# Kernel tuning notes

Measured on AMD Instinct MI355X. Metric: run time of the kernel, lower is better.

Reference implementation:

```python
import jax, jax.numpy as jnp
import numpy as np

N = 100000      # nodes
E = 1200000     # edges (every node gets >=1 incoming edge)
DIN = 64
DOUT = 64
EDIM = 16
AVG_D = 2.5649493574615367  # log(avg_in_degree + 1) = log(13)
EPS = 1e-5


def setup_inputs() -> dict:
    key = jax.random.key(0)
    ks = jax.random.split(key, 10)
    h = jax.random.normal(ks[0], (N, DIN), dtype=jnp.float32)
    e = jax.random.normal(ks[1], (E, EDIM), dtype=jnp.float32)
    snorm_n = jax.random.uniform(ks[2], (N, 1), dtype=jnp.float32, minval=0.05, maxval=1.0)
    src = jax.random.randint(ks[3], (E,), 0, N, dtype=jnp.int32)
    # guarantee in-degree >= 1 for every node (DGL reduce requires non-empty mailbox)
    dst = jnp.concatenate([jnp.arange(N, dtype=jnp.int32),
                           jax.random.randint(ks[4], (E - N,), 0, N, dtype=jnp.int32)])
    d_pre_in = 2 * DIN + EDIM  # 144
    d_post_in = (4 * 3 + 1) * DIN  # 832
    W_pre = jax.random.normal(ks[5], (d_pre_in, DIN), dtype=jnp.float32) / np.sqrt(d_pre_in)
    b_pre = jnp.zeros((DIN,), dtype=jnp.float32)
    W_post = jax.random.normal(ks[6], (d_post_in, DOUT), dtype=jnp.float32) / np.sqrt(d_post_in)
    b_post = jnp.zeros((DOUT,), dtype=jnp.float32)
    bn_gamma = jnp.ones((DOUT,), dtype=jnp.float32)
    bn_beta = jnp.zeros((DOUT,), dtype=jnp.float32)
    return {"h": h, "e": e, "snorm_n": snorm_n,
            "W_pre": W_pre, "b_pre": b_pre, "W_post": W_post, "b_post": b_post,
            "bn_gamma": bn_gamma, "bn_beta": bn_beta, "src": src, "dst": dst}


def reference(h, e, snorm_n, W_pre, b_pre, W_post, b_post, bn_gamma, bn_beta, src, dst):
    n = h.shape[0]
    # --- pretrans on edges: MLP(cat[src_feat, dst_feat, edge_feat]) (1 layer, no act) ---
    z = jnp.concatenate([h[src], h[dst], e], axis=1)           # [E, 2*DIN+EDIM]
    m = z @ W_pre + b_pre                                      # [E, DIN] edge messages
    # --- multi-aggregator segment reduce over destination mailboxes ---
    deg = jax.ops.segment_sum(jnp.ones((m.shape[0],), m.dtype), dst, num_segments=n)
    D = deg[:, None]                                           # [N,1], all >= 1
    s1 = jax.ops.segment_sum(m, dst, num_segments=n)
    s2 = jax.ops.segment_sum(m * m, dst, num_segments=n)
    mean = s1 / D
    std = jnp.sqrt(jax.nn.relu(s2 / D - mean * mean) + EPS)
    mx = jax.ops.segment_max(m, dst, num_segments=n)
    mn = jax.ops.segment_min(m, dst, num_segments=n)
    agg = jnp.concatenate([mean, mx, mn, std], axis=1)          # [N, 4*DIN]
    # --- degree scalers: identity, amplification, attenuation ---
    logd = jnp.log(D + 1.0)
    scaled = jnp.concatenate([agg, agg * (logd / AVG_D), agg * (AVG_D / logd)], axis=1)  # [N, 12*DIN]
    # --- posttrans on cat[h, aggregated] (1 layer, no act) ---
    feat = jnp.concatenate([h, scaled], axis=1)                 # [N, 13*DIN]
    out = feat @ W_post + b_post                                # [N, DOUT]
    out = out * snorm_n                                        # graph norm
    # BatchNorm1d in training mode (batch stats over nodes, biased var)
    mu = out.mean(axis=0)
    var = out.var(axis=0)
    out = (out - mu) / jnp.sqrt(var + 1e-5) * bn_gamma + bn_beta
    # dropout p=0.0 -> identity
    return out
```

## Files before the change

kernel.cpp:

```cpp
#include <hip/hip_runtime.h>
#include <hip/hip_bf16.h>
#include <math.h>

#define N_NODES 100000
#define N_EDGES 1200000
#define NT_EDGE 75000
#define NPASS   3
#define TILES_PER_PASS 25000
#define ROWS_PER_PASS  400000
#define NT_POST 6250
#define AVG_D   2.5649493574615367f
#define EPSV    1e-5f

#define BUK_SHIFT 9
#define NBUK 196
#define EB_PER_BLOCK 4096

typedef __attribute__((ext_vector_type(8))) short short8;
typedef __attribute__((ext_vector_type(4))) float f32x4;

struct ERec { unsigned eid, sn, dn; };

#define OFF_DEG       0u
#define OFF_ROWLOCAL  400000u
#define OFF_BSUM      800000u
#define OFF_BOFFS     802048u
#define OFF_ROWSTART  804096u
#define OFF_CURSOR    1204096u
#define OFF_EREC      1604096u
#define OFF_AB        16004096u
#define OFF_BNACC     16804096u
#define OFF_BNFIN     16804608u
#define OFF_HB        16805120u
#define OFF_MBUF      29605120u
#define OFF_AGG       80805120u
#define OFF_WFRAG     132005120u
#define OFF_WFRAG2    132025600u
#define OFF_CARRY     OFF_BSUM
#define OFF_STAGING   OFF_MBUF
#define OFF_OUTPRE    OFF_MBUF

__device__ __forceinline__ short f2b(float f){
    union { float f; unsigned u; } c; c.f = f;
    unsigned u = c.u;
    unsigned r = (u + 0x7fffu + ((u >> 16) & 1u)) >> 16;
    return (short)r;
}
__device__ __forceinline__ float b2f(unsigned u16){
    union { unsigned u; float f; } c; c.u = u16 << 16;
    return c.f;
}
__device__ __forceinline__ unsigned pk(float a, float b){
    return ((unsigned)(unsigned short)f2b(a)) | (((unsigned)(unsigned short)f2b(b)) << 16);
}

__global__ void k_prep(const int* __restrict__ dst, unsigned* __restrict__ deg,
                       const float* __restrict__ h, unsigned short* __restrict__ hb,
                       const float* __restrict__ W_pre, unsigned short* __restrict__ wfrag,
                       const float* __restrict__ W_post, unsigned short* __restrict__ wfrag2){
    int i = blockIdx.x*256 + threadIdx.x;
    if (i < N_EDGES) atomicAdd(&deg[dst[i]], 1u);
    if (i < 800000){
        const float4* p = (const float4*)h + (size_t)i*2;
        float4 u0 = p[0], u1 = p[1];
        uint4 o;
        o.x = pk(u0.x,u0.y); o.y = pk(u0.z,u0.w);
        o.z = pk(u1.x,u1.y); o.w = pk(u1.z,u1.w);
        ((uint4*)hb)[i] = o;
    }
    if (i < 10240){
        int e = i & 7, l = (i>>3) & 63, q = i>>9;
        int ks = q>>2, cg = q&3;
        int lr = l&15, lg = l>>4;
        int k = ks*32 + lg*8 + e, col = cg*16 + lr;
        wfrag[i] = (unsigned short)((k < 144) ? f2b(W_pre[k*64 + col]) : (short)0);
    }
    if (i < 53248){
        int e = i & 7, l = (i>>3) & 63, g = i>>9;
        int cg = g & 3, f = g>>2;
        int lr = l&15, lg = l>>4;
        int col = cg*16 + lr;
        int row;
        if      (f < 10) row = f*32        + lg*8 + e;
        else if (f < 18) row = 320 + (f-10)*32 + lg*8 + e;
        else             row = 576 + (f-18)*32 + lg*8 + e;
        wfrag2[i] = (unsigned short)f2b(W_post[row*64 + col]);
    }
}
__global__ void k_scan1(const unsigned* __restrict__ deg, unsigned* __restrict__ rowlocal,
                        unsigned* __restrict__ bsum){
    __shared__ unsigned s[256];
    int t = threadIdx.x; int i = blockIdx.x*256 + t;
    unsigned d = (i < N_NODES) ? deg[i] : 0u;
    s[t] = d; __syncthreads();
    for (int off=1; off<256; off<<=1){
        unsigned v = (t>=off) ? s[t-off] : 0u; __syncthreads();
        s[t] += v; __syncthreads();
    }
    if (i < N_NODES) rowlocal[i] = s[t] - d;
    if (t == 255) bsum[blockIdx.x] = s[255];
}
__global__ void k_scan2(const unsigned* __restrict__ bsum, unsigned* __restrict__ boffs){
    __shared__ unsigned s[512];
    int t = threadIdx.x;
    unsigned v = (t < 391) ? bsum[t] : 0u;
    s[t] = v; __syncthreads();
    for (int off=1; off<512; off<<=1){
        unsigned x = (t>=off) ? s[t-off] : 0u; __syncthreads();
        s[t] += x; __syncthreads();
    }
    boffs[t] = s[t] - v;
}
__global__ void k_scan3(const unsigned* __restrict__ rowlocal, const unsigned* __restrict__ boffs,
                        unsigned* __restrict__ rowstart, unsigned* __restrict__ bukCursor){
    int i = blockIdx.x*256 + threadIdx.x;
    if (i < N_NODES){
        unsigned v = rowlocal[i] + boffs[i>>8];
        rowstart[i] = v;
        if ((i & 511) == 0) bukCursor[i>>BUK_SHIFT] = v;
    }
}

__global__ __launch_bounds__(256) void k_bin(
    const int* __restrict__ src, const int* __restrict__ dst,
    unsigned* __restrict__ bukCursor, ERec* __restrict__ staging)
{
    __shared__ unsigned hist[NBUK];
    __shared__ unsigned gbase[NBUK];
    int tid = threadIdx.x;
    for (int j=tid; j<NBUK; j+=256) hist[j]=0u;
    __syncthreads();
    int base = blockIdx.x*EB_PER_BLOCK;
    int sn[16], dn[16];
    #pragma unroll
    for (int k=0;k<16;k++){
        int i = base + k*256 + tid;
        if (i < N_EDGES){
            sn[k]=src[i]; dn[k]=dst[i];
            atomicAdd(&hist[dn[k]>>BUK_SHIFT],1u);
        } else dn[k] = -1;
    }
    __syncthreads();
    for (int j=tid; j<NBUK; j+=256){
        unsigned c = hist[j];
        gbase[j] = c ? atomicAdd(&bukCursor[j], c) : 0u;
        hist[j] = 0u;
    }
    __syncthreads();
    #pragma unroll
    for (int k=0;k<16;k++){
        int i = base + k*256 + tid;
        if (i < N_EDGES){
            int b = dn[k]>>BUK_SHIFT;
            unsigned off = atomicAdd(&hist[b],1u);
            ERec r; r.eid=(unsigned)i; r.sn=(unsigned)sn[k]; r.dn=(unsigned)dn[k];
            staging[gbase[b]+off] = r;
        }
    }
}

__global__ __launch_bounds__(256) void k_place(
    const ERec* __restrict__ staging, const unsigned* __restrict__ rowstart,
    ERec* __restrict__ erec)
{
    __shared__ unsigned cur[512];
    int b = blockIdx.x;
    int nbase = b<<BUK_SHIFT;
    int nend  = nbase + 512; if (nend > N_NODES) nend = N_NODES;
    int tid = threadIdx.x;
    for (int j=tid; j<512; j+=256)
        cur[j] = (nbase+j < N_NODES) ? rowstart[nbase+j] : (unsigned)N_EDGES;
    __syncthreads();
    unsigned p0 = rowstart[nbase];
    unsigned p1 = (nend < N_NODES) ? rowstart[nend] : (unsigned)N_EDGES;
    for (unsigned p = p0 + tid; p < p1; p += 256){
        ERec r = staging[p];
        unsigned pos = atomicAdd(&cur[r.dn - nbase], 1u);
        erec[pos] = r;
    }
}

__global__ __launch_bounds__(256) void k_edge(
    const unsigned short* __restrict__ hb, const float* __restrict__ e_in,
    const unsigned short* __restrict__ wfrag, const float* __restrict__ b_pre,
    const ERec* __restrict__ erec, unsigned short* __restrict__ mbuf, int pass)
{
    __shared__ __align__(16) uint4 wfl[1280];
    int tid = threadIdx.x;
    int wv = tid>>6, l = tid&63;
    int lr = l&15, lg = l>>4;

    int t = blockIdx.x*4 + wv;
    const ERec* er = erec + (size_t)pass*ROWS_PER_PASS;
    ERec r = er[(size_t)t*16 + lr];

    for (int j=tid; j<1280; j+=256) wfl[j] = ((const uint4*)wfrag)[j];
    __syncthreads();

    const unsigned short* ps = hb + (size_t)r.sn*64 + lg*8;
    const unsigned short* pd = hb + (size_t)r.dn*64 + lg*8;
    short8 A[5];
    A[0] = *(const short8*)ps;
    A[1] = *(const short8*)(ps + 32);
    A[2] = *(const short8*)pd;
    A[3] = *(const short8*)(pd + 32);
    {
        short8 A4 = {0,0,0,0,0,0,0,0};
        if (lg < 2){
            const float* pe = e_in + (size_t)r.eid*16 + lg*8;
            float4 u0 = *(const float4*)pe, u1 = *(const float4*)(pe+4);
            A4[0]=f2b(u0.x); A4[1]=f2b(u0.y); A4[2]=f2b(u0.z); A4[3]=f2b(u0.w);
            A4[4]=f2b(u1.x); A4[5]=f2b(u1.y); A4[6]=f2b(u1.z); A4[7]=f2b(u1.w);
        }
        A[4] = A4;
    }

    f32x4 acc[4];
    #pragma unroll
    for (int cg=0; cg<4; cg++) acc[cg] = (f32x4){0.f,0.f,0.f,0.f};
    #pragma unroll
    for (int ks=0; ks<5; ks++){
        #pragma unroll
        for (int cg=0; cg<4; cg++){
            short8 b = ((const short8*)wfl)[(ks*4+cg)*64 + l];
            acc[cg] = __builtin_amdgcn_mfma_f32_16x16x32_bf16(A[ks], b, acc[cg], 0,0,0);
        }
    }
    float bias[4];
    #pragma unroll
    for (int cg=0; cg<4; cg++) bias[cg] = b_pre[cg*16 + lr];
    #pragma unroll
    for (int rr=0; rr<4; rr++){
        size_t row = (size_t)t*16 + lg*4 + rr;
        #pragma unroll
        for (int cg=0; cg<4; cg++)
            mbuf[row*64 + cg*16 + lr] = (unsigned short)f2b(acc[cg][rr] + bias[cg]);
    }
}

__global__ __launch_bounds__(256) void k_agg(
    const unsigned short* __restrict__ mbuf, const unsigned* __restrict__ rowstart,
    const unsigned* __restrict__ deg, unsigned short* __restrict__ agg,
    float* __restrict__ ab, float* __restrict__ carry, int pass)
{
    int wv = threadIdx.x>>6, l = threadIdx.x&63;
    int node = blockIdx.x*4 + wv;
    int hf = l>>5, c = l&31;
    unsigned start = rowstart[node];
    int d = (int)deg[node];
    unsigned end = start + (unsigned)d;
    unsigned lo = (unsigned)pass * ROWS_PER_PASS;
    unsigned hi = lo + ROWS_PER_PASS;
    if (end <= lo || start >= hi) return;
    unsigned a = start < lo ? lo : start;
    unsigned b = end > hi ? hi : end;
    int n = (int)(b - a);
    const unsigned short* p = mbuf + (size_t)(a - lo)*64 + 2*c;
    float s1a=0.f,s2a=0.f,mxa=-3.402823466e38f,mna=3.402823466e38f;
    float s1b=0.f,s2b=0.f,mxb=-3.402823466e38f,mnb=3.402823466e38f;
    for (int i=hf; i<n; i+=2){
        unsigned v = *(const unsigned*)(p + (size_t)i*64);
        float va = b2f(v & 0xffffu), vb = b2f(v >> 16);
        s1a += va; s2a = fmaf(va,va,s2a); mxa = fmaxf(mxa,va); mna = fminf(mna,va);
        s1b += vb; s2b = fmaf(vb,vb,s2b); mxb = fmaxf(mxb,vb); mnb = fminf(mnb,vb);
    }
    s1a += __shfl_xor(s1a,32); s2a += __shfl_xor(s2a,32);
    mxa = fmaxf(mxa,__shfl_xor(mxa,32)); mna = fminf(mna,__shfl_xor(mna,32));
    s1b += __shfl_xor(s1b,32); s2b += __shfl_xor(s2b,32);
    mxb = fmaxf(mxb,__shfl_xor(mxb,32)); mnb = fminf(mnb,__shfl_xor(mnb,32));
    if (l < 32){
        if (start < lo){
            const float* cb = carry + (size_t)(pass-1)*256;
            s1a += cb[      2*c];   s1b += cb[      2*c+1];
            s2a += cb[ 64 + 2*c];   s2b += cb[ 64 + 2*c+1];
            mxa = fmaxf(mxa, cb[128 + 2*c]); mxb = fmaxf(mxb, cb[128 + 2*c+1]);
            mna = fminf(mna, cb[192 + 2*c]); mnb = fminf(mnb, cb[192 + 2*c+1]);
        }
        if (end > hi){
            float* cb = carry + (size_t)pass*256;
            cb[      2*c] = s1a;  cb[      2*c+1] = s1b;
            cb[ 64 + 2*c] = s2a;  cb[ 64 + 2*c+1] = s2b;
            cb[128 + 2*c] = mxa;  cb[128 + 2*c+1] = mxb;
            cb[192 + 2*c] = mna;  cb[192 + 2*c+1] = mnb;
        } else {
            float D = (float)d;
            float meana = s1a/D, meanb = s1b/D;
            float sda = sqrtf(fmaxf(s2a/D - meana*meana, 0.f) + EPSV);
            float sdb = sqrtf(fmaxf(s2b/D - meanb*meanb, 0.f) + EPSV);
            unsigned* ag = (unsigned*)(agg + (size_t)node*256) + c;
            ag[ 0] = pk(meana, meanb);
            ag[32] = pk(mxa,  mxb);
            ag[64] = pk(mna,  mnb);
            ag[96] = pk(sda,  sdb);
            if (c == 0){
                float logd = logf(D + 1.f);
                ab[node*2]   = logd / AVG_D;
                ab[node*2+1] = AVG_D / logd;
            }
        }
    }
}

__global__ __launch_bounds__(256) void k_post(
    const unsigned short* __restrict__ hb, const unsigned short* __restrict__ agg,
    const unsigned short* __restrict__ wfrag2,
    const float* __restrict__ ab, const float* __restrict__ snorm,
    const float* __restrict__ b_post,
    float* __restrict__ out_pre, float* __restrict__ bn_acc)
{
    int tid = threadIdx.x;
    int cg = tid>>6;
    int l = tid&63, lr = l&15, lg = l>>4;
    int col = cg*16 + lr;

    const short8* wf = (const short8*)wfrag2;
    short8 Bm[10], B2[8], B3[8];
    #pragma unroll
    for (int ks=0; ks<10; ks++) Bm[ks] = wf[(ks*4      + cg)*64 + l];
    #pragma unroll
    for (int ks=0; ks<8; ks++){
        B2[ks] = wf[((10+ks)*4 + cg)*64 + l];
        B3[ks] = wf[((18+ks)*4 + cg)*64 + l];
    }
    float bias = b_post[col];
    float bs = 0.f, bq = 0.f;

    for (int t = blockIdx.x; t < NT_POST; t += gridDim.x){
        int nodeA = t*16 + lr;
        f32x4 aM = {0.f,0.f,0.f,0.f}, a2 = {0.f,0.f,0.f,0.f}, a3 = {0.f,0.f,0.f,0.f};
        #pragma unroll
        for (int ks=0; ks<2; ks++){
            short8 A = *(const short8*)(hb + (size_t)nodeA*64 + ks*32 + lg*8);
            aM = __builtin_amdgcn_mfma_f32_16x16x32_bf16(A, Bm[ks], aM, 0,0,0);
        }
        #pragma unroll
        for (int ks=0; ks<8; ks++){
            short8 A = *(const short8*)(agg + (size_t)nodeA*256 + ks*32 + lg*8);
            aM = __builtin_amdgcn_mfma_f32_16x16x32_bf16(A, Bm[2+ks], aM, 0,0,0);
            a2 = __builtin_amdgcn_mfma_f32_16x16x32_bf16(A, B2[ks],  a2, 0,0,0);
            a3 = __builtin_amdgcn_mfma_f32_16x16x32_bf16(A, B3[ks],  a3, 0,0,0);
        }
        #pragma unroll
        for (int r=0; r<4; r++){
            int node = t*16 + lg*4 + r;
            float av = ab[node*2], bv = ab[node*2+1];
            float v = (aM[r] + av*a2[r] + bv*a3[r] + bias) * snorm[node];
            out_pre[(size_t)node*64 + col] = v;
            bs += v; bq = fmaf(v,v,bq);
        }
    }
    bs += __shfl_xor(bs, 16); bs += __shfl_xor(bs, 32);
    bq += __shfl_xor(bq, 16); bq += __shfl_xor(bq, 32);
    if (l < 16){
        atomicAdd(&bn_acc[cg*16 + l], bs);
        atomicAdd(&bn_acc[64 + cg*16 + l], bq);
    }
}

__global__ void k_bnfin(const float* __restrict__ bn_acc, const float* __restrict__ gamma,
                        const float* __restrict__ beta, float* __restrict__ bn_fin){
    int c = threadIdx.x;
    float invN = 1.f/(float)N_NODES;
    float mu = bn_acc[c]*invN;
    float ms = bn_acc[64+c]*invN;
    float var = fmaxf(ms - mu*mu, 0.f);
    float scale = gamma[c] / sqrtf(var + 1e-5f);
    bn_fin[c] = scale;
    bn_fin[64+c] = beta[c] - mu*scale;
}
__global__ void k_apply(const float* __restrict__ out_pre, const float* __restrict__ bn_fin,
                        float* __restrict__ out){
    int i = blockIdx.x*256 + threadIdx.x;
    int c4 = (i & 15) * 4;
    float4 v  = ((const float4*)out_pre)[i];
    float4 sc = *(const float4*)&bn_fin[c4];
    float4 sh = *(const float4*)&bn_fin[64 + c4];
    float4 o;
    o.x = fmaf(v.x, sc.x, sh.x); o.y = fmaf(v.y, sc.y, sh.y);
    o.z = fmaf(v.z, sc.z, sh.z); o.w = fmaf(v.w, sc.w, sh.w);
    ((float4*)out)[i] = o;
}

extern "C" void kernel_launch(void* const* d_in, const int* in_sizes, int n_in,
                              void* d_out, int out_size, void* d_ws, size_t ws_size,
                              hipStream_t stream)
{
    const float* h      = (const float*)d_in[0];
    const float* e_in   = (const float*)d_in[1];
    const float* snorm  = (const float*)d_in[2];
    const float* W_pre  = (const float*)d_in[3];
    const float* b_pre  = (const float*)d_in[4];
    const float* W_post = (const float*)d_in[5];
    const float* b_post = (const float*)d_in[6];
    const float* gamma  = (const float*)d_in[7];
    const float* beta   = (const float*)d_in[8];
    const int*   src    = (const int*)d_in[9];
    const int*   dst    = (const int*)d_in[10];

    char* ws = (char*)d_ws;
    unsigned* deg      = (unsigned*)(ws + OFF_DEG);
    unsigned* rowlocal = (unsigned*)(ws + OFF_ROWLOCAL);
    unsigned* bsum     = (unsigned*)(ws + OFF_BSUM);
    unsigned* boffs    = (unsigned*)(ws + OFF_BOFFS);
    unsigned* rowstart = (unsigned*)(ws + OFF_ROWSTART);
    unsigned* bukCur   = (unsigned*)(ws + OFF_CURSOR);
    ERec*     erec     = (ERec*)(ws + OFF_EREC);
    ERec*     staging  = (ERec*)(ws + OFF_STAGING);
    float*    abuf     = (float*)(ws + OFF_AB);
    float*    bnacc    = (float*)(ws + OFF_BNACC);
    float*    bnfin    = (float*)(ws + OFF_BNFIN);
    unsigned short* hb     = (unsigned short*)(ws + OFF_HB);
    unsigned short* mbuf   = (unsigned short*)(ws + OFF_MBUF);
    unsigned short* aggp   = (unsigned short*)(ws + OFF_AGG);
    unsigned short* wfrag  = (unsigned short*)(ws + OFF_WFRAG);
    unsigned short* wfrag2 = (unsigned short*)(ws + OFF_WFRAG2);
    float*    carry    = (float*)(ws + OFF_CARRY);
    float*    outpre   = (float*)(ws + OFF_OUTPRE);

    hipMemsetAsync(ws + OFF_DEG,   0, 400000, stream);
    hipMemsetAsync(ws + OFF_BNACC, 0, 512,    stream);

    k_prep   <<<4688, 256, 0, stream>>>(dst, deg, h, hb, W_pre, wfrag, W_post, wfrag2);
    k_scan1  <<<391,  256, 0, stream>>>(deg, rowlocal, bsum);
    k_scan2  <<<1,    512, 0, stream>>>(bsum, boffs);
    k_scan3  <<<391,  256, 0, stream>>>(rowlocal, boffs, rowstart, bukCur);
    k_bin    <<<293,  256, 0, stream>>>(src, dst, bukCur, staging);
    k_place  <<<NBUK, 256, 0, stream>>>(staging, rowstart, erec);

    for (int pass = 0; pass < NPASS; pass++){
        k_edge <<<6250, 256, 0, stream>>>(hb, e_in, wfrag, b_pre, erec, mbuf, pass);
        k_agg  <<<25000,256, 0, stream>>>(mbuf, rowstart, deg, aggp, abuf, carry, pass);
    }

    k_post   <<<1024, 256, 0, stream>>>(hb, aggp, wfrag2, abuf, snorm, b_post, outpre, bnacc);
    k_bnfin  <<<1,    64,  0, stream>>>(bnacc, gamma, beta, bnfin);
    k_apply  <<<6250, 256, 0, stream>>>(outpre, bnfin, (float*)d_out);
}
```

Measured before the change: 479.5 us.

## Fuse edge message MLP with per-node aggregation, eliminating message buffer passes

The edge-message GEMM and the segment aggregation are merged into one persistent node-centric kernel. Each wave processes one destination node's mailbox in 16-edge MFMA tiles and reduces sum, sum-of-squares, max and min in registers. This removes the 3-pass write and read of a bf16 message buffer and the carry logic, and shrinks edge records to (eid, src). The post kernel now stages W_post fragments in shared memory per column group instead of holding them in registers. In exchange, tiles are partially empty for low-degree nodes (average about 12 edges), wasting MFMA work, and the dst-feature MFMAs are recomputed for every tile.

```diff
diff --git a/kernel.cpp b/kernel.cpp
--- a/kernel.cpp
+++ b/kernel.cpp
@@ -4,10 +4,6 @@
 
 #define N_NODES 100000
 #define N_EDGES 1200000
-#define NT_EDGE 75000
-#define NPASS   3
-#define TILES_PER_PASS 25000
-#define ROWS_PER_PASS  400000
 #define NT_POST 6250
 #define AVG_D   2.5649493574615367f
 #define EPSV    1e-5f
@@ -27,28 +23,22 @@
 #define OFF_BOFFS     802048u
 #define OFF_ROWSTART  804096u
 #define OFF_CURSOR    1204096u
-#define OFF_EREC      1604096u
-#define OFF_AB        16004096u
-#define OFF_BNACC     16804096u
-#define OFF_BNFIN     16804608u
-#define OFF_HB        16805120u
-#define OFF_MBUF      29605120u
-#define OFF_AGG       80805120u
-#define OFF_WFRAG     132005120u
-#define OFF_WFRAG2    132025600u
-#define OFF_CARRY     OFF_BSUM
-#define OFF_STAGING   OFF_MBUF
-#define OFF_OUTPRE    OFF_MBUF
+#define OFF_EREC      1205120u
+#define OFF_AB        10805120u
+#define OFF_BNACC     11605120u
+#define OFF_BNFIN     11605632u
+#define OFF_HB        11606144u
+#define OFF_AGG       24406144u
+#define OFF_WFRAG     75606144u
+#define OFF_WFRAG2    75626624u
+#define OFF_STAGING   75733120u
+#define OFF_OUTPRE    OFF_STAGING
 
 __device__ __forceinline__ short f2b(float f){
     union { float f; unsigned u; } c; c.f = f;
     unsigned u = c.u;
     unsigned r = (u + 0x7fffu + ((u >> 16) & 1u)) >> 16;
     return (short)r;
-}
-__device__ __forceinline__ float b2f(unsigned u16){
-    union { unsigned u; float f; } c; c.u = u16 << 16;
-    return c.f;
 }
 __device__ __forceinline__ unsigned pk(float a, float b){
     return ((unsigned)(unsigned short)f2b(a)) | (((unsigned)(unsigned short)f2b(b)) << 16);
@@ -161,7 +151,7 @@
 
 __global__ __launch_bounds__(256) void k_place(
     const ERec* __restrict__ staging, const unsigned* __restrict__ rowstart,
-    ERec* __restrict__ erec)
+    uint2* __restrict__ erec)
 {
     __shared__ unsigned cur[512];
     int b = blockIdx.x;
@@ -176,124 +166,100 @@
     for (unsigned p = p0 + tid; p < p1; p += 256){
         ERec r = staging[p];
         unsigned pos = atomicAdd(&cur[r.dn - nbase], 1u);
-        erec[pos] = r;
-    }
-}
-
-__global__ __launch_bounds__(256) void k_edge(
+        erec[pos] = make_uint2(r.eid, r.sn);
+    }
+}
+
+__global__ __launch_bounds__(256) void k_node(
     const unsigned short* __restrict__ hb, const float* __restrict__ e_in,
     const unsigned short* __restrict__ wfrag, const float* __restrict__ b_pre,
-    const ERec* __restrict__ erec, unsigned short* __restrict__ mbuf, int pass)
+    const uint2* __restrict__ erec, const unsigned* __restrict__ rowstart,
+    const unsigned* __restrict__ deg, unsigned short* __restrict__ agg,
+    float* __restrict__ ab)
 {
     __shared__ __align__(16) uint4 wfl[1280];
     int tid = threadIdx.x;
-    int wv = tid>>6, l = tid&63;
-    int lr = l&15, lg = l>>4;
-
-    int t = blockIdx.x*4 + wv;
-    const ERec* er = erec + (size_t)pass*ROWS_PER_PASS;
-    ERec r = er[(size_t)t*16 + lr];
-
+    int wv = tid>>6, l = tid&63, lr = l&15, lg = l>>4;
     for (int j=tid; j<1280; j+=256) wfl[j] = ((const uint4*)wfrag)[j];
     __syncthreads();
-
-    const unsigned short* ps = hb + (size_t)r.sn*64 + lg*8;
-    const unsigned short* pd = hb + (size_t)r.dn*64 + lg*8;
-    short8 A[5];
-    A[0] = *(const short8*)ps;
-    A[1] = *(const short8*)(ps + 32);
-    A[2] = *(const short8*)pd;
-    A[3] = *(const short8*)(pd + 32);
-    {
-        short8 A4 = {0,0,0,0,0,0,0,0};
-        if (lg < 2){
-            const float* pe = e_in + (size_t)r.eid*16 + lg*8;
-            float4 u0 = *(const float4*)pe, u1 = *(const float4*)(pe+4);
-            A4[0]=f2b(u0.x); A4[1]=f2b(u0.y); A4[2]=f2b(u0.z); A4[3]=f2b(u0.w);
-            A4[4]=f2b(u1.x); A4[5]=f2b(u1.y); A4[6]=f2b(u1.z); A4[7]=f2b(u1.w);
-        }
-        A[4] = A4;
-    }
-
-    f32x4 acc[4];
-    #pragma unroll
-    for (int cg=0; cg<4; cg++) acc[cg] = (f32x4){0.f,0.f,0.f,0.f};
-    #pragma unroll
-    for (int ks=0; ks<5; ks++){
-        #pragma unroll
-        for (int cg=0; cg<4; cg++){
-            short8 b = ((const short8*)wfl)[(ks*4+cg)*64 + l];
-            acc[cg] = __builtin_amdgcn_mfma_f32_16x16x32_bf16(A[ks], b, acc[cg], 0,0,0);
-        }
-    }
+    const short8* B = (const short8*)wfl;
     float bias[4];
     #pragma unroll
     for (int cg=0; cg<4; cg++) bias[cg] = b_pre[cg*16 + lr];
-    #pragma unroll
-    for (int rr=0; rr<4; rr++){
-        size_t row = (size_t)t*16 + lg*4 + rr;
-        #pragma unroll
-        for (int cg=0; cg<4; cg++)
-            mbuf[row*64 + cg*16 + lr] = (unsigned short)f2b(acc[cg][rr] + bias[cg]);
-    }
-}
-
-__global__ __launch_bounds__(256) void k_agg(
-    const unsigned short* __restrict__ mbuf, const unsigned* __restrict__ rowstart,
-    const unsigned* __restrict__ deg, unsigned short* __restrict__ agg,
-    float* __restrict__ ab, float* __restrict__ carry, int pass)
-{
-    int wv = threadIdx.x>>6, l = threadIdx.x&63;
-    int node = blockIdx.x*4 + wv;
-    int hf = l>>5, c = l&31;
-    unsigned start = rowstart[node];
-    int d = (int)deg[node];
-    unsigned end = start + (unsigned)d;
-    unsigned lo = (unsigned)pass * ROWS_PER_PASS;
-    unsigned hi = lo + ROWS_PER_PASS;
-    if (end <= lo || start >= hi) return;
-    unsigned a = start < lo ? lo : start;
-    unsigned b = end > hi ? hi : end;
-    int n = (int)(b - a);
-    const unsigned short* p = mbuf + (size_t)(a - lo)*64 + 2*c;
-    float s1a=0.f,s2a=0.f,mxa=-3.402823466e38f,mna=3.402823466e38f;
-    float s1b=0.f,s2b=0.f,mxb=-3.402823466e38f,mnb=3.402823466e38f;
-    for (int i=hf; i<n; i+=2){
-        unsigned v = *(const unsigned*)(p + (size_t)i*64);
-        float va = b2f(v & 0xffffu), vb = b2f(v >> 16);
-        s1a += va; s2a = fmaf(va,va,s2a); mxa = fmaxf(mxa,va); mna = fminf(mna,va);
-        s1b += vb; s2b = fmaf(vb,vb,s2b); mxb = fmaxf(mxb,vb); mnb = fminf(mnb,vb);
-    }
-    s1a += __shfl_xor(s1a,32); s2a += __shfl_xor(s2a,32);
-    mxa = fmaxf(mxa,__shfl_xor(mxa,32)); mna = fminf(mna,__shfl_xor(mna,32));
-    s1b += __shfl_xor(s1b,32); s2b += __shfl_xor(s2b,32);
-    mxb = fmaxf(mxb,__shfl_xor(mxb,32)); mnb = fminf(mnb,__shfl_xor(mnb,32));
-    if (l < 32){
-        if (start < lo){
-            const float* cb = carry + (size_t)(pass-1)*256;
-            s1a += cb[      2*c];   s1b += cb[      2*c+1];
-            s2a += cb[ 64 + 2*c];   s2b += cb[ 64 + 2*c+1];
-            mxa = fmaxf(mxa, cb[128 + 2*c]); mxb = fmaxf(mxb, cb[128 + 2*c+1]);
-            mna = fminf(mna, cb[192 + 2*c]); mnb = fminf(mnb, cb[192 + 2*c+1]);
-        }
-        if (end > hi){
-            float* cb = carry + (size_t)pass*256;
-            cb[      2*c] = s1a;  cb[      2*c+1] = s1b;
-            cb[ 64 + 2*c] = s2a;  cb[ 64 + 2*c+1] = s2b;
-            cb[128 + 2*c] = mxa;  cb[128 + 2*c+1] = mxb;
-            cb[192 + 2*c] = mna;  cb[192 + 2*c+1] = mnb;
-        } else {
-            float D = (float)d;
-            float meana = s1a/D, meanb = s1b/D;
-            float sda = sqrtf(fmaxf(s2a/D - meana*meana, 0.f) + EPSV);
-            float sdb = sqrtf(fmaxf(s2b/D - meanb*meanb, 0.f) + EPSV);
-            unsigned* ag = (unsigned*)(agg + (size_t)node*256) + c;
-            ag[ 0] = pk(meana, meanb);
-            ag[32] = pk(mxa,  mxb);
-            ag[64] = pk(mna,  mnb);
-            ag[96] = pk(sda,  sdb);
-            if (c == 0){
-                float logd = logf(D + 1.f);
+
+    for (int node = blockIdx.x*4 + wv; node < N_NODES; node += gridDim.x*4){
+        unsigned start = rowstart[node];
+        int d = (int)deg[node];
+        const unsigned short* pn = hb + (size_t)node*64 + lg*8;
+        short8 D0 = *(const short8*)pn;
+        short8 D1 = *(const short8*)(pn + 32);
+        float s1[4], s2[4], mx[4], mn[4];
+        #pragma unroll
+        for (int cg=0; cg<4; cg++){
+            s1[cg]=0.f; s2[cg]=0.f; mx[cg]=-3.402823466e38f; mn[cg]=3.402823466e38f;
+        }
+        for (int base=0; base<d; base+=16){
+            int rem = d - base;
+            short8 A0={0,0,0,0,0,0,0,0}, A1={0,0,0,0,0,0,0,0}, A4={0,0,0,0,0,0,0,0};
+            if (lr < rem){
+                uint2 er = erec[start + base + lr];
+                const unsigned short* ps = hb + (size_t)er.y*64 + lg*8;
+                A0 = *(const short8*)ps;
+                A1 = *(const short8*)(ps + 32);
+                if (lg < 2){
+                    const float* pe = e_in + (size_t)er.x*16 + lg*8;
+                    float4 u0 = *(const float4*)pe, u1 = *(const float4*)(pe+4);
+                    A4[0]=f2b(u0.x); A4[1]=f2b(u0.y); A4[2]=f2b(u0.z); A4[3]=f2b(u0.w);
+                    A4[4]=f2b(u1.x); A4[5]=f2b(u1.y); A4[6]=f2b(u1.z); A4[7]=f2b(u1.w);
+                }
+            }
+            f32x4 acc[4];
+            #pragma unroll
+            for (int cg=0; cg<4; cg++) acc[cg] = (f32x4){0.f,0.f,0.f,0.f};
+            #pragma unroll
+            for (int cg=0; cg<4; cg++) acc[cg] = __builtin_amdgcn_mfma_f32_16x16x32_bf16(A0, B[(0*4+cg)*64+l], acc[cg], 0,0,0);
+            #pragma unroll
+            for (int cg=0; cg<4; cg++) acc[cg] = __builtin_amdgcn_mfma_f32_16x16x32_bf16(A1, B[(1*4+cg)*64+l], acc[cg], 0,0,0);
+            #pragma unroll
+            for (int cg=0; cg<4; cg++) acc[cg] = __builtin_amdgcn_mfma_f32_16x16x32_bf16(D0, B[(2*4+cg)*64+l], acc[cg], 0,0,0);
+            #pragma unroll
+            for (int cg=0; cg<4; cg++) acc[cg] = __builtin_amdgcn_mfma_f32_16x16x32_bf16(D1, B[(3*4+cg)*64+l], acc[cg], 0,0,0);
+            #pragma unroll
+            for (int cg=0; cg<4; cg++) acc[cg] = __builtin_amdgcn_mfma_f32_16x16x32_bf16(A4, B[(4*4+cg)*64+l], acc[cg], 0,0,0);
+            #pragma unroll
+            for (int rr=0; rr<4; rr++){
+                bool v = (base + lg*4 + rr) < d;
+                #pragma unroll
+                for (int cg=0; cg<4; cg++){
+                    float m = acc[cg][rr] + bias[cg];
+                    if (v){
+                        s1[cg] += m; s2[cg] = fmaf(m,m,s2[cg]);
+                        mx[cg] = fmaxf(mx[cg],m); mn[cg] = fminf(mn[cg],m);
+                    }
+                }
+            }
+        }
+        #pragma unroll
+        for (int cg=0; cg<4; cg++){
+            s1[cg] += __shfl_xor(s1[cg],16); s1[cg] += __shfl_xor(s1[cg],32);
+            s2[cg] += __shfl_xor(s2[cg],16); s2[cg] += __shfl_xor(s2[cg],32);
+            mx[cg] = fmaxf(mx[cg],__shfl_xor(mx[cg],16)); mx[cg] = fmaxf(mx[cg],__shfl_xor(mx[cg],32));
+            mn[cg] = fminf(mn[cg],__shfl_xor(mn[cg],16)); mn[cg] = fminf(mn[cg],__shfl_xor(mn[cg],32));
+        }
+        if (l < 16){
+            float Dv = (float)d;
+            unsigned short* ag = agg + (size_t)node*256;
+            #pragma unroll
+            for (int cg=0; cg<4; cg++){
+                float mean = s1[cg]/Dv;
+                float sd = sqrtf(fmaxf(s2[cg]/Dv - mean*mean, 0.f) + EPSV);
+                ag[      cg*16 + lr] = (unsigned short)f2b(mean);
+                ag[ 64 + cg*16 + lr] = (unsigned short)f2b(mx[cg]);
+                ag[128 + cg*16 + lr] = (unsigned short)f2b(mn[cg]);
+                ag[192 + cg*16 + lr] = (unsigned short)f2b(sd);
+            }
+            if (l == 0){
+                float logd = logf(Dv + 1.f);
                 ab[node*2]   = logd / AVG_D;
                 ab[node*2+1] = AVG_D / logd;
             }
@@ -308,37 +274,35 @@
     const float* __restrict__ b_post,
     float* __restrict__ out_pre, float* __restrict__ bn_acc)
 {
+    __shared__ __align__(16) uint4 wfs[1664];
     int tid = threadIdx.x;
-    int cg = tid>>6;
-    int l = tid&63, lr = l&15, lg = l>>4;
+    int cg = blockIdx.x & 3;
+    int bg = blockIdx.x >> 2;
+    int wv = tid>>6, l = tid&63, lr = l&15, lg = l>>4;
+    for (int j=tid; j<1664; j+=256){
+        int f = j>>6, ll = j&63;
+        wfs[j] = ((const uint4*)wfrag2)[(size_t)(f*4 + cg)*64 + ll];
+    }
+    __syncthreads();
+    const short8* B = (const short8*)wfs;
     int col = cg*16 + lr;
-
-    const short8* wf = (const short8*)wfrag2;
-    short8 Bm[10], B2[8], B3[8];
-    #pragma unroll
-    for (int ks=0; ks<10; ks++) Bm[ks] = wf[(ks*4      + cg)*64 + l];
-    #pragma unroll
-    for (int ks=0; ks<8; ks++){
-        B2[ks] = wf[((10+ks)*4 + cg)*64 + l];
-        B3[ks] = wf[((18+ks)*4 + cg)*64 + l];
-    }
     float bias = b_post[col];
     float bs = 0.f, bq = 0.f;
 
-    for (int t = blockIdx.x; t < NT_POST; t += gridDim.x){
+    for (int t = bg*4 + wv; t < NT_POST; t += 1564){
         int nodeA = t*16 + lr;
         f32x4 aM = {0.f,0.f,0.f,0.f}, a2 = {0.f,0.f,0.f,0.f}, a3 = {0.f,0.f,0.f,0.f};
         #pragma unroll
         for (int ks=0; ks<2; ks++){
             short8 A = *(const short8*)(hb + (size_t)nodeA*64 + ks*32 + lg*8);
-            aM = __builtin_amdgcn_mfma_f32_16x16x32_bf16(A, Bm[ks], aM, 0,0,0);
+            aM = __builtin_amdgcn_mfma_f32_16x16x32_bf16(A, B[ks*64 + l], aM, 0,0,0);
         }
         #pragma unroll
         for (int ks=0; ks<8; ks++){
             short8 A = *(const short8*)(agg + (size_t)nodeA*256 + ks*32 + lg*8);
-            aM = __builtin_amdgcn_mfma_f32_16x16x32_bf16(A, Bm[2+ks], aM, 0,0,0);
-            a2 = __builtin_amdgcn_mfma_f32_16x16x32_bf16(A, B2[ks],  a2, 0,0,0);
-            a3 = __builtin_amdgcn_mfma_f32_16x16x32_bf16(A, B3[ks],  a3, 0,0,0);
+            aM = __builtin_amdgcn_mfma_f32_16x16x32_bf16(A, B[( 2+ks)*64 + l], aM, 0,0,0);
+            a2 = __builtin_amdgcn_mfma_f32_16x16x32_bf16(A, B[(10+ks)*64 + l], a2, 0,0,0);
+            a3 = __builtin_amdgcn_mfma_f32_16x16x32_bf16(A, B[(18+ks)*64 + l], a3, 0,0,0);
         }
         #pragma unroll
         for (int r=0; r<4; r++){
@@ -352,8 +316,8 @@
     bs += __shfl_xor(bs, 16); bs += __shfl_xor(bs, 32);
     bq += __shfl_xor(bq, 16); bq += __shfl_xor(bq, 32);
     if (l < 16){
-        atomicAdd(&bn_acc[cg*16 + l], bs);
-        atomicAdd(&bn_acc[64 + cg*16 + l], bq);
+        atomicAdd(&bn_acc[col], bs);
+        atomicAdd(&bn_acc[64 + col], bq);
     }
 }
 
@@ -404,17 +368,15 @@
     unsigned* boffs    = (unsigned*)(ws + OFF_BOFFS);
     unsigned* rowstart = (unsigned*)(ws + OFF_ROWSTART);
     unsigned* bukCur   = (unsigned*)(ws + OFF_CURSOR);
-    ERec*     erec     = (ERec*)(ws + OFF_EREC);
+    uint2*    erec     = (uint2*)(ws + OFF_EREC);
     ERec*     staging  = (ERec*)(ws + OFF_STAGING);
     float*    abuf     = (float*)(ws + OFF_AB);
     float*    bnacc    = (float*)(ws + OFF_BNACC);
     float*    bnfin    = (float*)(ws + OFF_BNFIN);
     unsigned short* hb     = (unsigned short*)(ws + OFF_HB);
-    unsigned short* mbuf   = (unsigned short*)(ws + OFF_MBUF);
     unsigned short* aggp   = (unsigned short*)(ws + OFF_AGG);
     unsigned short* wfrag  = (unsigned short*)(ws + OFF_WFRAG);
     unsigned short* wfrag2 = (unsigned short*)(ws + OFF_WFRAG2);
-    float*    carry    = (float*)(ws + OFF_CARRY);
     float*    outpre   = (float*)(ws + OFF_OUTPRE);
 
     hipMemsetAsync(ws + OFF_DEG,   0, 400000, stream);
@@ -427,12 +389,9 @@
     k_bin    <<<293,  256, 0, stream>>>(src, dst, bukCur, staging);
     k_place  <<<NBUK, 256, 0, stream>>>(staging, rowstart, erec);
 
-    for (int pass = 0; pass < NPASS; pass++){
-        k_edge <<<6250, 256, 0, stream>>>(hb, e_in, wfrag, b_pre, erec, mbuf, pass);
-        k_agg  <<<25000,256, 0, stream>>>(mbuf, rowstart, deg, aggp, abuf, carry, pass);
-    }
-
-    k_post   <<<1024, 256, 0, stream>>>(hb, aggp, wfrag2, abuf, snorm, b_post, outpre, bnacc);
+    k_node   <<<3125, 256, 0, stream>>>(hb, e_in, wfrag, b_pre, erec, rowstart, deg, aggp, abuf);
+
+    k_post   <<<1564, 256, 0, stream>>>(hb, aggp, wfrag2, abuf, snorm, b_post, outpre, bnacc);
     k_bnfin  <<<1,    64,  0, stream>>>(bnacc, gamma, beta, bnfin);
     k_apply  <<<6250, 256, 0, stream>>>(outpre, bnfin, (float*)d_out);
 }
```

New measurement: 541.0 us. +12.8%, slower.
